# Performance work log

Hardware: AMD Instinct MI355X
Metric: run time of the kernel (lower is better)

## Reference

```python
import jax, jax.numpy as jnp
import numpy as np


def _sobel(img):
    # replicate-pad then Sobel cross-correlation (matches torch conv2d with wx, wy)
    p = jnp.pad(img, ((0, 0), (0, 0), (1, 1), (1, 1)), mode='edge')
    dx = ((p[:, :, 0:-2, 2:] - p[:, :, 0:-2, 0:-2])
          + 2.0 * (p[:, :, 1:-1, 2:] - p[:, :, 1:-1, 0:-2])
          + (p[:, :, 2:, 2:] - p[:, :, 2:, 0:-2]))
    dy = ((p[:, :, 2:, 0:-2] - p[:, :, 0:-2, 0:-2])
          + 2.0 * (p[:, :, 2:, 1:-1] - p[:, :, 0:-2, 1:-1])
          + (p[:, :, 2:, 2:] - p[:, :, 0:-2, 2:]))
    return dx, dy


def _compute_normal(vertex):
    # normal = normalize(dV/dx x dV/dy); zero out pixels at global min/max depth
    dx, dy = _sobel(vertex)
    n = jnp.cross(dx, dy, axis=1)                      # [B,3,H,W]
    mag = jnp.sqrt(jnp.sum(n * n, axis=1, keepdims=True) + 1e-16)
    n = n / (mag + 1e-8)
    depth = vertex[:, 2:3]
    invalid = (depth == depth.min()) | (depth == depth.max())
    return jnp.where(invalid, 0.0, n)


def _warp(feat, u, v):
    # bilinear sampling of feat [B,C,H,W] at (u,v) [B,N] -> [B,C,N]
    B, C, H, W = feat.shape
    u = jnp.clip(u, 0.0, W - 1.0)
    v = jnp.clip(v, 0.0, H - 1.0)
    u0 = jnp.floor(u); v0 = jnp.floor(v)
    wu = u - u0; wv = v - v0
    u0i = u0.astype(jnp.int32); v0i = v0.astype(jnp.int32)
    u1i = jnp.minimum(u0i + 1, W - 1); v1i = jnp.minimum(v0i + 1, H - 1)
    flat = feat.reshape(B, C, H * W)
    N = u.shape[-1]
    def g(ui, vi):
        idx = (vi * W + ui)[:, None, :]
        return jnp.take_along_axis(flat, jnp.broadcast_to(idx, (B, C, N)), axis=2)
    return (g(u0i, v0i) * ((1 - wu) * (1 - wv))[:, None]
            + g(u1i, v0i) * (wu * (1 - wv))[:, None]
            + g(u0i, v1i) * ((1 - wu) * wv)[:, None]
            + g(u1i, v1i) * (wu * wv)[:, None])


def _skew(v):  # [B,3] -> [B,3,3]
    x, y, z = v[..., 0], v[..., 1], v[..., 2]
    O = jnp.zeros_like(x)
    return jnp.stack([jnp.stack([O, -z, y], -1),
                      jnp.stack([z, O, -x], -1),
                      jnp.stack([-y, x, O], -1)], -2)


def _twist2mat(w):  # Rodrigues: so(3) [B,3] -> SO(3) [B,3,3]
    th = jnp.sqrt(jnp.sum(w * w, -1, keepdims=True) + 1e-24)
    Kv = _skew(w / th)
    th = th[..., None]
    I = jnp.eye(3, dtype=w.dtype)
    return I + jnp.sin(th) * Kv + (1.0 - jnp.cos(th)) * (Kv @ Kv)


def _icp_forward(depth0, depth1, K, R, t, max_iter=3):
    B, _, H, W = depth0.shape
    fx, fy, cx, cy = [K[:, i:i + 1] for i in range(4)]  # each [B,1]
    uu = jnp.arange(W, dtype=depth0.dtype)
    vv = jnp.arange(H, dtype=depth0.dtype)
    px = (uu[None, None, None, :] - cx[:, :, None, None]) / fx[:, :, None, None]
    py = (vv[None, None, :, None] - cy[:, :, None, None]) / fy[:, :, None, None]
    px = jnp.broadcast_to(px, (B, 1, H, W))
    py = jnp.broadcast_to(py, (B, 1, H, W))
    vertex0 = jnp.concatenate([px * depth0, py * depth0, depth0], 1)  # [B,3,H,W]
    vertex1 = jnp.concatenate([px * depth1, py * depth1, depth1], 1)
    normal0 = _compute_normal(vertex0)
    normal1 = _compute_normal(vertex1)
    N = H * W
    V0 = vertex0.reshape(B, 3, N)
    N0 = normal0.reshape(B, 3, N)
    P0 = V0.transpose(0, 2, 1)                          # [B,N,3]
    dpt0 = vertex0[:, 2].reshape(B, N)
    sigma_z = 0.0012 + 0.0019 * (dpt0 - 0.4) ** 2       # depth noise model
    eye6 = jnp.eye(6, dtype=depth0.dtype)
    for _ in range(max_iter):
        v0to1 = R @ V0 + t                               # [B,3,N]
        x_, y_, s_ = v0to1[:, 0], v0to1[:, 1], v0to1[:, 2]
        u_ = x_ / s_ * fx + cx
        v_ = y_ / s_ * fy + cy
        inviews = (u_ > 0) & (u_ < W - 1) & (v_ > 0) & (v_ < H - 1)
        rV1 = _warp(vertex1, u_, v_)                     # [B,3,N]
        rN1 = _warp(normal1, u_, v_)
        diff = v0to1 - rV1
        dnorm = jnp.sqrt(jnp.sum(diff * diff, axis=1) + 1e-16)
        occ = (~inviews) | (dnorm > 0.1)                 # [B,N]
        res = jnp.sum(rN1 * diff, axis=1)                # point-to-plane residual [B,N]
        NtC = jnp.einsum('bcn,bck->bnk', rN1, R)         # n_r^T R, [B,N,3]
        # n^T [p]_x == cross(n^T R, p)
        J = jnp.concatenate([jnp.cross(NtC, P0), -NtC], -1)  # [B,N,6]
        # sigma ~ |n_r . (R e_z)| * sigma_z (depth noise projected on normal)
        ndot = jnp.abs(jnp.sum(rN1 * R[:, :, 2][:, :, None], axis=1))
        sigma = ndot * sigma_z + 1e-3
        w_res = res / (sigma + 1e-8)
        J = -J / (sigma + 1e-8)[..., None]
        w_res = jnp.where(occ, 0.0, w_res)
        J = jnp.where(occ[..., None], 0.0, J)
        JtWJ = jnp.einsum('bnk,bnl->bkl', J, J)          # [B,6,6]
        JtR = jnp.einsum('bnk,bn->bk', J, w_res)[..., None]  # [B,6,1]
        tr = jnp.trace(JtWJ, axis1=1, axis2=2)
        Hlm = JtWJ + (tr * 1e-6)[:, None, None] * eye6   # LM damping
        xi = jnp.linalg.inv(Hlm) @ JtR                   # [B,6,1]
        dR = _twist2mat(-xi[:, :3, 0])
        dt = -(dR @ xi[:, 3:])
        R, t = R @ dR, R @ dt + t                        # inverse-compositional update
    weights = jnp.ones((B, 1, H, W), dtype=depth0.dtype)
    return R, t, weights


def setup_inputs() -> dict:
    key = jax.random.key(0)
    B, H, W = 16, 480, 640
    k1, k2, k3, k4 = jax.random.split(key, 4)
    TWO_PI = 6.2831853
    xs = jnp.linspace(0.0, 1.0, W, dtype=jnp.float32)
    ys = jnp.linspace(0.0, 1.0, H, dtype=jnp.float32)
    phase = jax.random.uniform(k1, (B, 1, 1, 1), minval=0.0, maxval=TWO_PI)
    # smooth positive depth surface so ICP inlier test keeps valid pixels
    depth0 = (2.0 + 0.5 * jnp.sin(TWO_PI * 3.0 * xs[None, None, None, :] + phase)
              * jnp.cos(TWO_PI * 2.0 * ys[None, None, :, None])).astype(jnp.float32)
    depth1 = depth0 + 0.01 * jax.random.normal(k2, (B, 1, H, W), dtype=jnp.float32)
    K = jnp.tile(jnp.array([[525.0, 525.0, 319.5, 239.5]], dtype=jnp.float32), (B, 1))
    w = 0.005 * jax.random.normal(k3, (B, 3), dtype=jnp.float32)
    R = _twist2mat(w)                                    # near-identity initial rotation
    t = 0.005 * jax.random.normal(k4, (B, 3, 1), dtype=jnp.float32)
    return {"depth0": depth0, "depth1": depth1, "K": K, "R": R, "t": t}


def reference(depth0, depth1, K, R, t):
    return _icp_forward(depth0, depth1, K, R, t, max_iter=3)
```

## Files before the change

kernel.cpp:

```cpp
#include <hip/hip_runtime.h>

#define IMH 480
#define IMW 640
#define HW (IMH*IMW)
#define NB 16

#define BPB 150
#define TPX 4
#define GROUPS 2
#define THREADS_PB (BPB*256)
#define GSTRIDE (THREADS_PB*TPX)
#define GROWS (GSTRIDE/IMW)

__device__ inline unsigned fenc(float x){
    unsigned u = __float_as_uint(x);
    return (u & 0x80000000u) ? ~u : (u | 0x80000000u);
}
__device__ inline float fdec(unsigned e){
    unsigned u = (e & 0x80000000u) ? (e & 0x7FFFFFFFu) : ~e;
    return __uint_as_float(u);
}

__global__ void init_kernel(const float* __restrict__ Rin, const float* __restrict__ tin,
                            float* __restrict__ stateR, float* __restrict__ statet,
                            unsigned* __restrict__ mm, float* __restrict__ acc){
    int i = threadIdx.x;
    if (i < NB*9) stateR[i] = Rin[i];
    if (i < NB*3) statet[i] = tin[i];
    if (i == 0){ mm[0] = 0xFFFFFFFFu; mm[1] = 0u; }
    for (int k = i; k < NB*27; k += 256) acc[k] = 0.f;
}

__global__ __launch_bounds__(256) void minmax_kernel(const float4* __restrict__ d, unsigned* __restrict__ mm){
    unsigned lmin = 0xFFFFFFFFu, lmax = 0u;
    const int total4 = NB*HW/4;
    for (int i = blockIdx.x*256 + threadIdx.x; i < total4; i += gridDim.x*256){
        float4 v = d[i];
        unsigned e0 = fenc(v.x), e1 = fenc(v.y), e2 = fenc(v.z), e3 = fenc(v.w);
        lmin = min(lmin, min(min(e0,e1), min(e2,e3)));
        lmax = max(lmax, max(max(e0,e1), max(e2,e3)));
    }
    #pragma unroll
    for (int off = 32; off; off >>= 1){
        lmin = min(lmin, (unsigned)__shfl_down((int)lmin, off));
        lmax = max(lmax, (unsigned)__shfl_down((int)lmax, off));
    }
    __shared__ unsigned smin[4], smax[4];
    int wave = threadIdx.x >> 6, lane = threadIdx.x & 63;
    if (lane == 0){ smin[wave] = lmin; smax[wave] = lmax; }
    __syncthreads();
    if (threadIdx.x == 0){
        unsigned bmin = min(min(smin[0],smin[1]), min(smin[2],smin[3]));
        unsigned bmax = max(max(smax[0],smax[1]), max(smax[2],smax[3]));
        atomicMin(&mm[0], bmin);
        atomicMax(&mm[1], bmax);
    }
}

__global__ __launch_bounds__(256) void normal_kernel(const float* __restrict__ depth1,
                                                     const float* __restrict__ Kp,
                                                     const unsigned* __restrict__ mm,
                                                     uint4* __restrict__ nrm4,
                                                     float4* __restrict__ weights4){
    const int b = blockIdx.y;
    const int t = blockIdx.x*256 + threadIdx.x;
    const int gpr = IMW/4;
    const int r = t / gpr;
    const int c0 = (t - r*gpr)*4;
    const float fx = Kp[b*4+0], fy = Kp[b*4+1], cx = Kp[b*4+2], cy = Kp[b*4+3];
    const float inv_fx = 1.f/fx, inv_fy = 1.f/fy;
    const float* __restrict__ d = depth1 + (size_t)b*HW;
    const int rm = max(r-1,0), rp = min(r+1,IMH-1);

    float wm[6], wc[6], wp[6];
    {
        const float* rowm = d + rm*IMW + c0;
        const float* rowc = d + r *IMW + c0;
        const float* rowp = d + rp*IMW + c0;
        float4 vm = *(const float4*)rowm;
        float4 vc = *(const float4*)rowc;
        float4 vp = *(const float4*)rowp;
        wm[1]=vm.x; wm[2]=vm.y; wm[3]=vm.z; wm[4]=vm.w;
        wc[1]=vc.x; wc[2]=vc.y; wc[3]=vc.z; wc[4]=vc.w;
        wp[1]=vp.x; wp[2]=vp.y; wp[3]=vp.z; wp[4]=vp.w;
        bool hasL = (c0 > 0), hasR = (c0+4 < IMW);
        wm[0] = hasL ? rowm[-1] : vm.x;   wm[5] = hasR ? rowm[4] : vm.w;
        wc[0] = hasL ? rowc[-1] : vc.x;   wc[5] = hasR ? rowc[4] : vc.w;
        wp[0] = hasL ? rowp[-1] : vp.x;   wp[5] = hasR ? rowp[4] : vp.w;
    }
    float pxw[6];
    #pragma unroll
    for (int k=0;k<6;k++){
        int cc = min(max(c0-1+k, 0), IMW-1);
        pxw[k] = ((float)cc - cx)*inv_fx;
    }
    const float pym = ((float)rm - cy)*inv_fy;
    const float pyc = ((float)r  - cy)*inv_fy;
    const float pyp = ((float)rp - cy)*inv_fy;

    const float dmin = fdec(mm[0]), dmax = fdec(mm[1]);

    unsigned packed[4];
    #pragma unroll
    for (int j=0;j<4;j++){
        float aL = wm[j],  aC = wm[j+1], aR = wm[j+2];
        float bL = wc[j],               bR = wc[j+2];
        float cL = wp[j],  cC = wp[j+1], cR = wp[j+2];
        float pL = pxw[j], pC = pxw[j+1], pR = pxw[j+2];

        float dx0 = (pR*aR - pL*aL) + 2.f*(pR*bR - pL*bL) + (pR*cR - pL*cL);
        float dx1 = pym*(aR - aL) + 2.f*pyc*(bR - bL) + pyp*(cR - cL);
        float dx2 = (aR - aL) + 2.f*(bR - bL) + (cR - cL);
        float dy0 = pL*(cL - aL) + 2.f*pC*(cC - aC) + pR*(cR - aR);
        float dy1 = (pyp*cL - pym*aL) + 2.f*(pyp*cC - pym*aC) + (pyp*cR - pym*aR);
        float dy2 = (cL - aL) + 2.f*(cC - aC) + (cR - aR);

        float nx = dx1*dy2 - dx2*dy1;
        float ny = dx2*dy0 - dx0*dy2;
        float nz = dx0*dy1 - dx1*dy0;
        float mag = sqrtf(nx*nx + ny*ny + nz*nz + 1e-16f);
        float inv = __builtin_amdgcn_rcpf(mag + 1e-8f);
        nx *= inv; ny *= inv; nz *= inv;

        float dc = wc[j+1];
        if (dc == dmin || dc == dmax){ nx = 0.f; ny = 0.f; nz = 0.f; }

        int qx = (int)rintf(nx*127.f) + 127;
        int qy = (int)rintf(ny*127.f) + 127;
        int qz = (int)rintf(nz*127.f) + 127;
        packed[j] = ((unsigned)qx) | ((unsigned)qy << 8) | ((unsigned)qz << 16);
    }

    size_t o4 = (size_t)b*(HW/4) + (size_t)r*gpr + (c0>>2);
    nrm4[o4] = make_uint4(packed[0], packed[1], packed[2], packed[3]);
    weights4[o4] = make_float4(1.f,1.f,1.f,1.f);
}

__global__ __launch_bounds__(256) void iter_kernel(const float4* __restrict__ depth0_v4,
                                                   const float* __restrict__ depth1,
                                                   const unsigned* __restrict__ nrm,
                                                   const float* __restrict__ Kp,
                                                   const float* __restrict__ stateR,
                                                   const float* __restrict__ statet,
                                                   float* __restrict__ acc){
    const int b = blockIdx.y;
    const float fx = Kp[b*4+0], fy = Kp[b*4+1], cx = Kp[b*4+2], cy = Kp[b*4+3];
    const float inv_fx = 1.f/fx, inv_fy = 1.f/fy;
    float Rm[9];
    #pragma unroll
    for (int i=0;i<9;i++) Rm[i] = stateR[b*9+i];
    float tv[3];
    #pragma unroll
    for (int i=0;i<3;i++) tv[i] = statet[b*3+i];

    const float4* __restrict__ d0v = depth0_v4 + (size_t)b*(HW/4);
    const float* __restrict__ d1   = depth1 + (size_t)b*HW;
    const unsigned* __restrict__ nb_ = nrm + (size_t)b*HW;

    float accv[27];
    #pragma unroll
    for (int i=0;i<27;i++) accv[i] = 0.f;

    const int tid = blockIdx.x*256 + threadIdx.x;
    const int base0 = tid*TPX;
    const int c0 = base0 % IMW;
    const int r0 = base0 / IMW;
    const float px_base = ((float)c0 - cx)*inv_fx;
    float pyv = ((float)r0 - cy)*inv_fy;
    const float py_step = (float)GROWS*inv_fy;
    const float inv127 = 1.f/127.f;

    #pragma unroll 1
    for (int g = 0; g < GROUPS; g++){
        float4 d4 = d0v[tid + g*THREADS_PB];
        float dd[4] = {d4.x, d4.y, d4.z, d4.w};

        #pragma unroll
        for (int j = 0; j < TPX; j++){
            float d0 = dd[j];
            float V0x = (px_base + (float)j*inv_fx)*d0;
            float V0y = pyv*d0;
            float V0z = d0;

            float X = Rm[0]*V0x + Rm[1]*V0y + Rm[2]*V0z + tv[0];
            float Y = Rm[3]*V0x + Rm[4]*V0y + Rm[5]*V0z + tv[1];
            float Z = Rm[6]*V0x + Rm[7]*V0y + Rm[8]*V0z + tv[2];
            float invZ = __builtin_amdgcn_rcpf(Z);
            float uu = X*invZ*fx + cx;
            float vv = Y*invZ*fy + cy;

            bool inview = (uu > 0.f) && (uu < (float)(IMW-1)) && (vv > 0.f) && (vv < (float)(IMH-1));

            float J0=0.f,J1=0.f,J2=0.f,J3=0.f,J4=0.f,J5=0.f,wres=0.f;
            if (inview){
                float u0f = floorf(uu), v0f = floorf(vv);
                int u0 = (int)u0f, v0 = (int)v0f;
                float wu = uu - u0f, wv = vv - v0f;
                float w00 = (1.f-wu)*(1.f-wv), w10 = wu*(1.f-wv), w01 = (1.f-wu)*wv, w11 = wu*wv;
                int i00 = v0*IMW + u0;

                float d00 = d1[i00], d10 = d1[i00+1], d01 = d1[i00+IMW], d11 = d1[i00+IMW+1];
                unsigned h00 = nb_[i00], h10 = nb_[i00+1], h01 = nb_[i00+IMW], h11 = nb_[i00+IMW+1];

                float pxa = (u0f - cx)*inv_fx, pxb = pxa + inv_fx;
                float pya = (v0f - cy)*inv_fy, pyb = pya + inv_fy;
                float a = w00*d00, bb = w10*d10, cc = w01*d01, ee = w11*d11;
                float rVz = (a + bb) + (cc + ee);
                float rVx = (a + cc)*pxa + (bb + ee)*pxb;
                float rVy = (a + bb)*pya + (cc + ee)*pyb;

                float q00x = (float)(h00 & 0xFFu);
                float q00y = (float)((h00 >> 8) & 0xFFu);
                float q00z = (float)((h00 >> 16) & 0xFFu);
                float q10x = (float)(h10 & 0xFFu);
                float q10y = (float)((h10 >> 8) & 0xFFu);
                float q10z = (float)((h10 >> 16) & 0xFFu);
                float q01x = (float)(h01 & 0xFFu);
                float q01y = (float)((h01 >> 8) & 0xFFu);
                float q01z = (float)((h01 >> 16) & 0xFFu);
                float q11x = (float)(h11 & 0xFFu);
                float q11y = (float)((h11 >> 8) & 0xFFu);
                float q11z = (float)((h11 >> 16) & 0xFFu);

                float n0x = ((w00*q00x + w10*q10x + w01*q01x + w11*q11x) - 127.f) * inv127;
                float n0y = ((w00*q00y + w10*q10y + w01*q01y + w11*q11y) - 127.f) * inv127;
                float n0z = ((w00*q00z + w10*q10z + w01*q01z + w11*q11z) - 127.f) * inv127;

                float dfx = X - rVx, dfy = Y - rVy, dfz = Z - rVz;
                float d2 = dfx*dfx + dfy*dfy + dfz*dfz + 1e-16f;
                if (d2 <= 0.01f){
                    float res = n0x*dfx + n0y*dfy + n0z*dfz;
                    float N0 = n0x*Rm[0] + n0y*Rm[3] + n0z*Rm[6];
                    float N1 = n0x*Rm[1] + n0y*Rm[4] + n0z*Rm[7];
                    float N2 = n0x*Rm[2] + n0y*Rm[5] + n0z*Rm[8];
                    float cr0 = N1*V0z - N2*V0y;
                    float cr1 = N2*V0x - N0*V0z;
                    float cr2 = N0*V0y - N1*V0x;
                    float ndot = fabsf(N2);
                    float dsh = d0 - 0.4f;
                    float sigz = 0.0012f + 0.0019f*dsh*dsh;
                    float sigma = ndot*sigz + 0.001f;
                    float invs = __builtin_amdgcn_rcpf(sigma + 1e-8f);
                    wres = res*invs;
                    J0 = -cr0*invs; J1 = -cr1*invs; J2 = -cr2*invs;
                    J3 =  N0*invs;  J4 =  N1*invs;  J5 =  N2*invs;
                }
            }

            float Jv[6] = {J0,J1,J2,J3,J4,J5};
            int idx = 0;
            #pragma unroll
            for (int k=0;k<6;k++)
                #pragma unroll
                for (int l=k;l<6;l++){ accv[idx] += Jv[k]*Jv[l]; idx++; }
            #pragma unroll
            for (int k=0;k<6;k++){ accv[idx] += Jv[k]*wres; idx++; }
        }

        pyv += py_step;
    }

    #pragma unroll
    for (int i=0;i<27;i++){
        float v = accv[i];
        #pragma unroll
        for (int off=32; off; off >>= 1) v += __shfl_down(v, off);
        accv[i] = v;
    }

    __shared__ float sacc[4][27];
    int wave = threadIdx.x >> 6, lane = threadIdx.x & 63;
    if (lane == 0){
        #pragma unroll
        for (int i=0;i<27;i++) sacc[wave][i] = accv[i];
    }
    __syncthreads();
    if (threadIdx.x < 27){
        float s = sacc[0][threadIdx.x] + sacc[1][threadIdx.x]
                + sacc[2][threadIdx.x] + sacc[3][threadIdx.x];
        atomicAdd(&acc[b*27 + threadIdx.x], s);
    }
}

__global__ void solve_kernel(float* __restrict__ acc,
                             float* __restrict__ stateR, float* __restrict__ statet,
                             float* __restrict__ outR, float* __restrict__ outt){
    int b = threadIdx.x;
    if (b >= NB) return;

    float a27[27];
    #pragma unroll
    for (int i=0;i<27;i++) a27[i] = acc[b*27+i];
    #pragma unroll
    for (int i=0;i<27;i++) acc[b*27+i] = 0.f;

    float A[6][6], rhs[6];
    int idx = 0;
    #pragma unroll
    for (int k=0;k<6;k++)
        #pragma unroll
        for (int l=k;l<6;l++){ A[k][l] = a27[idx]; A[l][k] = a27[idx]; idx++; }
    #pragma unroll
    for (int k=0;k<6;k++) rhs[k] = a27[21+k];

    float tr = 0.f;
    #pragma unroll
    for (int k=0;k<6;k++) tr += A[k][k];
    float lm = tr*1e-6f;
    #pragma unroll
    for (int k=0;k<6;k++) A[k][k] += lm;

    float L[6][6];
    #pragma unroll
    for (int i=0;i<6;i++){
        #pragma unroll
        for (int j=0;j<=i;j++){
            float s = A[i][j];
            #pragma unroll
            for (int k=0;k<j;k++) s -= L[i][k]*L[j][k];
            if (i == j) L[i][i] = sqrtf(s);
            else        L[i][j] = s / L[j][j];
        }
    }
    float y[6];
    #pragma unroll
    for (int i=0;i<6;i++){
        float s = rhs[i];
        #pragma unroll
        for (int k=0;k<i;k++) s -= L[i][k]*y[k];
        y[i] = s / L[i][i];
    }
    float xi[6];
    #pragma unroll
    for (int ii=5; ii>=0; ii--){
        float s = y[ii];
        #pragma unroll
        for (int k=ii+1;k<6;k++) s -= L[k][ii]*xi[k];
        xi[ii] = s / L[ii][ii];
    }

    float w0 = -xi[0], w1 = -xi[1], w2 = -xi[2];
    float th = sqrtf(w0*w0 + w1*w1 + w2*w2 + 1e-24f);
    float ith = 1.f/th;
    float kx = w0*ith, ky = w1*ith, kz = w2*ith;
    float s = sinf(th), cm1 = 1.f - cosf(th);
    float dRm[9];
    dRm[0] = 1.f + cm1*(-ky*ky - kz*kz);
    dRm[1] = -s*kz + cm1*(kx*ky);
    dRm[2] =  s*ky + cm1*(kx*kz);
    dRm[3] =  s*kz + cm1*(kx*ky);
    dRm[4] = 1.f + cm1*(-kx*kx - kz*kz);
    dRm[5] = -s*kx + cm1*(ky*kz);
    dRm[6] = -s*ky + cm1*(kx*kz);
    dRm[7] =  s*kx + cm1*(ky*kz);
    dRm[8] = 1.f + cm1*(-kx*kx - ky*ky);

    float dt0 = -(dRm[0]*xi[3] + dRm[1]*xi[4] + dRm[2]*xi[5]);
    float dt1 = -(dRm[3]*xi[3] + dRm[4]*xi[4] + dRm[5]*xi[5]);
    float dt2 = -(dRm[6]*xi[3] + dRm[7]*xi[4] + dRm[8]*xi[5]);

    float Rm[9], tv[3];
    #pragma unroll
    for (int i=0;i<9;i++) Rm[i] = stateR[b*9+i];
    #pragma unroll
    for (int i=0;i<3;i++) tv[i] = statet[b*3+i];

    float Rn[9];
    #pragma unroll
    for (int i=0;i<3;i++)
        #pragma unroll
        for (int j=0;j<3;j++)
            Rn[i*3+j] = Rm[i*3+0]*dRm[0*3+j] + Rm[i*3+1]*dRm[1*3+j] + Rm[i*3+2]*dRm[2*3+j];
    float tn0 = Rm[0]*dt0 + Rm[1]*dt1 + Rm[2]*dt2 + tv[0];
    float tn1 = Rm[3]*dt0 + Rm[4]*dt1 + Rm[5]*dt2 + tv[1];
    float tn2 = Rm[6]*dt0 + Rm[7]*dt1 + Rm[8]*dt2 + tv[2];

    #pragma unroll
    for (int i=0;i<9;i++){ stateR[b*9+i] = Rn[i]; outR[b*9+i] = Rn[i]; }
    statet[b*3+0] = tn0; outt[b*3+0] = tn0;
    statet[b*3+1] = tn1; outt[b*3+1] = tn1;
    statet[b*3+2] = tn2; outt[b*3+2] = tn2;
}

extern "C" void kernel_launch(void* const* d_in, const int* in_sizes, int n_in,
                              void* d_out, int out_size, void* d_ws, size_t ws_size,
                              hipStream_t stream){
    const float* depth0 = (const float*)d_in[0];
    const float* depth1 = (const float*)d_in[1];
    const float* Kp     = (const float*)d_in[2];
    const float* Rin    = (const float*)d_in[3];
    const float* tin    = (const float*)d_in[4];

    float* out     = (float*)d_out;
    float* outR    = out;
    float* outt    = out + NB*9;
    float* weights = out + NB*12;

    unsigned* nrm  = (unsigned*)d_ws;
    float* stateR  = (float*)(nrm + (size_t)NB*HW);
    float* statet  = stateR + NB*9;
    unsigned* mm   = (unsigned*)(statet + NB*3);
    float* acc     = (float*)(mm + 2);

    init_kernel<<<1, 256, 0, stream>>>(Rin, tin, stateR, statet, mm, acc);
    minmax_kernel<<<dim3(256), 256, 0, stream>>>((const float4*)depth1, mm);
    normal_kernel<<<dim3(HW/4/256, NB), 256, 0, stream>>>(depth1, Kp, mm, (uint4*)nrm, (float4*)weights);
    for (int it = 0; it < 3; it++){
        iter_kernel<<<dim3(BPB, NB), 256, 0, stream>>>((const float4*)depth0, depth1, nrm, Kp, stateR, statet, acc);
        solve_kernel<<<1, 64, 0, stream>>>(acc, stateR, statet, outR, outt);
    }
}
```

Baseline: 246.9 us.

## Remove init kernel and global atomics; reduce min/max partials in normal kernel

```diff
diff --git a/kernel.cpp b/kernel.cpp
--- a/kernel.cpp
+++ b/kernel.cpp
@@ -5,13 +5,15 @@
 #define HW (IMH*IMW)
 #define NB 16
 
-#define BPB 150
+#define BPB 100
 #define TPX 4
-#define GROUPS 2
+#define GROUPS 3
 #define THREADS_PB (BPB*256)
 #define GSTRIDE (THREADS_PB*TPX)
 #define GROWS (GSTRIDE/IMW)
 
+#define MMB 256
+
 __device__ inline unsigned fenc(float x){
     unsigned u = __float_as_uint(x);
     return (u & 0x80000000u) ? ~u : (u | 0x80000000u);
@@ -21,20 +23,16 @@
     return __uint_as_float(u);
 }
 
-__global__ void init_kernel(const float* __restrict__ Rin, const float* __restrict__ tin,
-                            float* __restrict__ stateR, float* __restrict__ statet,
-                            unsigned* __restrict__ mm, float* __restrict__ acc){
-    int i = threadIdx.x;
-    if (i < NB*9) stateR[i] = Rin[i];
-    if (i < NB*3) statet[i] = tin[i];
-    if (i == 0){ mm[0] = 0xFFFFFFFFu; mm[1] = 0u; }
-    for (int k = i; k < NB*27; k += 256) acc[k] = 0.f;
-}
-
-__global__ __launch_bounds__(256) void minmax_kernel(const float4* __restrict__ d, unsigned* __restrict__ mm){
+__global__ __launch_bounds__(256) void minmax_kernel(const float4* __restrict__ d,
+                                                     unsigned* __restrict__ pmin,
+                                                     unsigned* __restrict__ pmax,
+                                                     float* __restrict__ acc){
+    if (blockIdx.x == 0){
+        for (int k = threadIdx.x; k < NB*27; k += 256) acc[k] = 0.f;
+    }
     unsigned lmin = 0xFFFFFFFFu, lmax = 0u;
     const int total4 = NB*HW/4;
-    for (int i = blockIdx.x*256 + threadIdx.x; i < total4; i += gridDim.x*256){
+    for (int i = blockIdx.x*256 + threadIdx.x; i < total4; i += MMB*256){
         float4 v = d[i];
         unsigned e0 = fenc(v.x), e1 = fenc(v.y), e2 = fenc(v.z), e3 = fenc(v.w);
         lmin = min(lmin, min(min(e0,e1), min(e2,e3)));
@@ -50,18 +48,38 @@
     if (lane == 0){ smin[wave] = lmin; smax[wave] = lmax; }
     __syncthreads();
     if (threadIdx.x == 0){
-        unsigned bmin = min(min(smin[0],smin[1]), min(smin[2],smin[3]));
-        unsigned bmax = max(max(smax[0],smax[1]), max(smax[2],smax[3]));
-        atomicMin(&mm[0], bmin);
-        atomicMax(&mm[1], bmax);
+        pmin[blockIdx.x] = min(min(smin[0],smin[1]), min(smin[2],smin[3]));
+        pmax[blockIdx.x] = max(max(smax[0],smax[1]), max(smax[2],smax[3]));
     }
 }
 
 __global__ __launch_bounds__(256) void normal_kernel(const float* __restrict__ depth1,
                                                      const float* __restrict__ Kp,
-                                                     const unsigned* __restrict__ mm,
+                                                     const unsigned* __restrict__ pmin,
+                                                     const unsigned* __restrict__ pmax,
                                                      uint4* __restrict__ nrm4,
                                                      float4* __restrict__ weights4){
+    __shared__ unsigned sred[8];
+    __shared__ unsigned sfin[2];
+    {
+        unsigned vmin = pmin[threadIdx.x];
+        unsigned vmax = pmax[threadIdx.x];
+        #pragma unroll
+        for (int off = 32; off; off >>= 1){
+            vmin = min(vmin, (unsigned)__shfl_down((int)vmin, off));
+            vmax = max(vmax, (unsigned)__shfl_down((int)vmax, off));
+        }
+        int wave = threadIdx.x >> 6, lane = threadIdx.x & 63;
+        if (lane == 0){ sred[wave] = vmin; sred[4+wave] = vmax; }
+        __syncthreads();
+        if (threadIdx.x == 0){
+            sfin[0] = min(min(sred[0],sred[1]), min(sred[2],sred[3]));
+            sfin[1] = max(max(sred[4],sred[5]), max(sred[6],sred[7]));
+        }
+        __syncthreads();
+    }
+    const float dmin = fdec(sfin[0]), dmax = fdec(sfin[1]);
+
     const int b = blockIdx.y;
     const int t = blockIdx.x*256 + threadIdx.x;
     const int gpr = IMW/4;
@@ -97,8 +115,6 @@
     const float pym = ((float)rm - cy)*inv_fy;
     const float pyc = ((float)r  - cy)*inv_fy;
     const float pyp = ((float)rp - cy)*inv_fy;
-
-    const float dmin = fdec(mm[0]), dmax = fdec(mm[1]);
 
     unsigned packed[4];
     #pragma unroll
@@ -283,6 +299,7 @@
 }
 
 __global__ void solve_kernel(float* __restrict__ acc,
+                             const float* __restrict__ prevR, const float* __restrict__ prevT,
                              float* __restrict__ stateR, float* __restrict__ statet,
                              float* __restrict__ outR, float* __restrict__ outt){
     int b = threadIdx.x;
@@ -361,9 +378,9 @@
 
     float Rm[9], tv[3];
     #pragma unroll
-    for (int i=0;i<9;i++) Rm[i] = stateR[b*9+i];
-    #pragma unroll
-    for (int i=0;i<3;i++) tv[i] = statet[b*3+i];
+    for (int i=0;i<9;i++) Rm[i] = prevR[b*9+i];
+    #pragma unroll
+    for (int i=0;i<3;i++) tv[i] = prevT[b*3+i];
 
     float Rn[9];
     #pragma unroll
@@ -397,16 +414,18 @@
     float* weights = out + NB*12;
 
     unsigned* nrm  = (unsigned*)d_ws;
-    float* stateR  = (float*)(nrm + (size_t)NB*HW);
+    unsigned* pmin = nrm + (size_t)NB*HW;
+    unsigned* pmax = pmin + MMB;
+    float* stateR  = (float*)(pmax + MMB);
     float* statet  = stateR + NB*9;
-    unsigned* mm   = (unsigned*)(statet + NB*3);
-    float* acc     = (float*)(mm + 2);
-
-    init_kernel<<<1, 256, 0, stream>>>(Rin, tin, stateR, statet, mm, acc);
-    minmax_kernel<<<dim3(256), 256, 0, stream>>>((const float4*)depth1, mm);
-    normal_kernel<<<dim3(HW/4/256, NB), 256, 0, stream>>>(depth1, Kp, mm, (uint4*)nrm, (float4*)weights);
+    float* acc     = statet + NB*3;
+
+    minmax_kernel<<<dim3(MMB), 256, 0, stream>>>((const float4*)depth1, pmin, pmax, acc);
+    normal_kernel<<<dim3(HW/4/256, NB), 256, 0, stream>>>(depth1, Kp, pmin, pmax, (uint4*)nrm, (float4*)weights);
     for (int it = 0; it < 3; it++){
-        iter_kernel<<<dim3(BPB, NB), 256, 0, stream>>>((const float4*)depth0, depth1, nrm, Kp, stateR, statet, acc);
-        solve_kernel<<<1, 64, 0, stream>>>(acc, stateR, statet, outR, outt);
-    }
-}
+        const float* Rsrc = (it == 0) ? Rin : stateR;
+        const float* tsrc = (it == 0) ? tin : statet;
+        iter_kernel<<<dim3(BPB, NB), 256, 0, stream>>>((const float4*)depth0, depth1, nrm, Kp, Rsrc, tsrc, acc);
+        solve_kernel<<<1, 64, 0, stream>>>(acc, Rsrc, tsrc, stateR, statet, outR, outt);
+    }
+}
```

Result: faster. 231.4 us (-6.3%).
